# Kernel optimization log

Measured on AMD Instinct MI355X. Metric: run time of the kernel, lower is better.

## Reference

```python
import jax, jax.numpy as jnp
import numpy as np

B, T, N = 4, 24, 512
IN_FT, HID1, HID2, OUT = 64, 64, 64, 64


def _gconv(A, v, W1, W2):
    # two stacked graph-conv layers: relu(A @ v @ W1) then A @ . @ W2 (pre-gate, linear)
    h = jax.nn.relu(jnp.einsum('bij,bjd->bid', A, v) @ W1)   # [B,N,HID2]
    return jnp.einsum('bij,bjd->bid', A, h) @ W2             # [B,N,OUT]


def setup_inputs() -> dict:
    key = jax.random.key(0)
    ks = jax.random.split(key, 10)
    d_in = HID1 + OUT
    def w(k, shape, fan_in):
        return jax.random.normal(k, shape, dtype=jnp.float32) / np.sqrt(fan_in)
    return {
        'x': jax.random.normal(ks[0], (B, T, N, IN_FT), dtype=jnp.float32),
        'e': jax.random.uniform(ks[1], (B, T, N, N, 1), dtype=jnp.float32),
        'fc_w': w(ks[2], (IN_FT, HID1), IN_FT),
        'fc_b': jnp.zeros((HID1,), dtype=jnp.float32),
        'Wz1': w(ks[3], (d_in, HID2), d_in), 'Wz2': w(ks[4], (HID2, OUT), HID2),
        'Wr1': w(ks[5], (d_in, HID2), d_in), 'Wr2': w(ks[6], (HID2, OUT), HID2),
        'Wc1': w(ks[7], (d_in, HID2), d_in), 'Wc2': w(ks[8], (HID2, OUT), HID2),
    }


def reference(x, e, fc_w, fc_b, Wz1, Wz2, Wr1, Wr2, Wc1, Wc2):
    # input projection: relu(Linear(in_ft -> hid_ft1))
    xp = jax.nn.relu(x @ fc_w + fc_b)            # [B,T,N,HID1]
    A = e[..., 0]                                # [B,T,N,N] edge weights
    h0 = jnp.zeros((B, N, OUT), dtype=x.dtype)

    def step(h, inp):
        xt, At = inp                             # [B,N,HID1], [B,N,N]
        xh = jnp.concatenate([xt, h], axis=-1)
        z = jax.nn.sigmoid(_gconv(At, xh, Wz1, Wz2))
        r = jax.nn.sigmoid(_gconv(At, xh, Wr1, Wr2))
        c = jnp.tanh(_gconv(At, jnp.concatenate([xt, r * h], axis=-1), Wc1, Wc2))
        hn = z * h + (1.0 - z) * c
        return hn, hn

    xs = (jnp.moveaxis(xp, 1, 0), jnp.moveaxis(A, 1, 0))  # time-major for scan
    _, hs = jax.lax.scan(step, h0, xs)            # [T,B,N,OUT]
    return jnp.moveaxis(hs, 0, 1)                 # [B,T,N,OUT]
```

## Files before the change

kernel.cpp:

```cpp
#include <hip/hip_runtime.h>
#include <cstdint>
#include <cstddef>

#define B_ 4
#define T_ 24
#define N_ 512

__device__ __forceinline__ float fsig(float x)  { return (float)(1.0 / (1.0 + exp(-(double)x))); }
__device__ __forceinline__ float ftanh(float x) { return (float)tanh((double)x); }

__device__ __forceinline__ int swz16(int f) { return (((f & 15) ^ ((f >> 4) & 15)) << 2); }


__global__ __launch_bounds__(256) void xpT_kernel(const float* __restrict__ x,
                                                  const float* __restrict__ fc_w,
                                                  const float* __restrict__ fc_b,
                                                  float* __restrict__ xpT) {
    __shared__ __align__(16) float sX[64 * 68];
    __shared__ __align__(16) float sW[64 * 64];
    __shared__ float sB[64];
    const int bt = blockIdx.y;
    const int n0 = blockIdx.x * 64;
    const int tid = threadIdx.x;
    for (int i = tid * 4; i < 4096; i += 1024)
        *(float4*)&sW[i] = *(const float4*)&fc_w[i];
    if (tid < 64) sB[tid] = fc_b[tid];
    {
        int r = tid >> 2, kq = (tid & 3) * 16;
        const float* p = x + ((size_t)bt * N_ + n0 + r) * 64 + kq;
        #pragma unroll
        for (int j = 0; j < 4; ++j)
            *(float4*)&sX[r * 68 + kq + j * 4] = *(const float4*)(p + j * 4);
    }
    __syncthreads();
    const int f = tid & 63, ng = tid >> 6;
    float d[16];
    #pragma unroll
    for (int j = 0; j < 16; ++j) d[j] = 0.f;
    for (int k = 0; k < 64; ++k) {
        float w = sW[k * 64 + f];
        #pragma unroll
        for (int j = 0; j < 16; ++j)
            d[j] = fmaf(sX[(ng * 16 + j) * 68 + k], w, d[j]);
    }
    const float bias = sB[f];
    float* o = xpT + ((size_t)bt * 64 + f) * N_ + n0 + ng * 16;
    #pragma unroll
    for (int j = 0; j < 16; ++j)
        o[j] = fmaxf(__fadd_rn(d[j], bias), 0.f);
}

__global__ __launch_bounds__(256) void ux_kernel(const float* __restrict__ e,
                                                 const float* __restrict__ xpT,
                                                 float* __restrict__ UX) {
    __shared__ __align__(16) float sA[2][64 * 72];
    __shared__ __align__(16) float sV[2][64 * 64];
    const int bt = blockIdx.y;
    const int m0 = blockIdx.x * 64;
    const int tid = threadIdx.x;
    const float* Ab = e + ((size_t)bt * N_ + m0) * N_;
    const float* s0 = xpT + (size_t)bt * 64 * N_;

    auto stageA = [&](float* dst, int kt) {
        const int r = tid >> 2, kq = (tid & 3) * 16;
        const float* src = Ab + (size_t)r * N_ + kt * 64 + kq;
        float* d = dst + r * 72 + kq;
        #pragma unroll
        for (int j = 0; j < 4; ++j)
            *(float4*)(d + j * 4) = *(const float4*)(src + j * 4);
    };
    auto stageV = [&](float* dst, int kt) {
        const int f = tid >> 2, q = tid & 3;
        const int sw = swz16(f);
        const float* src = s0 + (size_t)f * N_ + kt * 64;
        #pragma unroll
        for (int j = 0; j < 4; ++j) {
            int k = q * 16 + j * 4;
            *(float4*)&dst[f * 64 + (k ^ sw)] = *(const float4*)(src + k);
        }
    };

    stageA(sA[0], 0);
    stageV(sV[0], 0);
    __syncthreads();

    const int cg = tid & 15, rg = tid >> 4;
    const int c0 = cg * 4;
    float acc[4][4];
    #pragma unroll
    for (int i = 0; i < 4; ++i)
        #pragma unroll
        for (int j = 0; j < 4; ++j) acc[i][j] = 0.f;

    for (int kb = 0; kb < 8; ++kb) {
        if (kb < 7) { stageA(sA[(kb + 1) & 1], kb + 1); stageV(sV[(kb + 1) & 1], kb + 1); }
        const float* Ab_ = sA[kb & 1];
        const float* Vb_ = sV[kb & 1];
        #pragma unroll 4
        for (int kg = 0; kg < 16; ++kg) {
            const int k = kg * 4;
            float4 v[4], a[4];
            #pragma unroll
            for (int j = 0; j < 4; ++j)
                v[j] = *(const float4*)&Vb_[(c0 + j) * 64 + (k ^ swz16(c0 + j))];
            #pragma unroll
            for (int i = 0; i < 4; ++i)
                a[i] = *(const float4*)&Ab_[(rg * 4 + i) * 72 + k];
            #pragma unroll
            for (int i = 0; i < 4; ++i)
                #pragma unroll
                for (int j = 0; j < 4; ++j) {
                    acc[i][j] = fmaf(a[i].x, v[j].x, acc[i][j]);
                    acc[i][j] = fmaf(a[i].y, v[j].y, acc[i][j]);
                    acc[i][j] = fmaf(a[i].z, v[j].z, acc[i][j]);
                    acc[i][j] = fmaf(a[i].w, v[j].w, acc[i][j]);
                }
        }
        __syncthreads();
    }
    #pragma unroll
    for (int i = 0; i < 4; ++i)
        *(float4*)&UX[((size_t)bt * N_ + m0 + rg * 4 + i) * 64 + c0] =
            make_float4(acc[i][0], acc[i][1], acc[i][2], acc[i][3]);
}

template <int STAGE>
__global__ __launch_bounds__(256) void stage9_kernel(
    const float* __restrict__ e, int t,
    const float* __restrict__ UX,
    const float* __restrict__ Wz1, const float* __restrict__ Wz2,
    const float* __restrict__ Wr1, const float* __restrict__ Wr2,
    const float* __restrict__ Wc1, const float* __restrict__ Wc2,
    float* __restrict__ hT, float* __restrict__ hzT, float* __restrict__ hrT,
    float* __restrict__ zT, float* __restrict__ rhT, float* __restrict__ hcT,
    float* __restrict__ out)
{
    constexpr int F = (STAGE == 2) ? 128 : 64;
    constexpr int SC = F + 4;
    __shared__ __align__(16) float sA[8 * 512];
    __shared__ __align__(16) float sV[2 * F * 64];
    __shared__ __align__(16) float sC[8 * SC];
    __shared__ __align__(16) float sUX[8 * 68];

    const int b = blockIdx.y;
    const int m0 = blockIdx.x * 8;
    const int tid = threadIdx.x;
    const int bt = b * T_ + t;

    const float* Ab = e + ((size_t)bt * N_ + m0) * N_;

    const float* s0;
    const float* s1 = nullptr;
    if (STAGE == 1)      { s0 = hT  + (size_t)b * 64 * N_; }
    else if (STAGE == 2) { s0 = hzT + (size_t)b * 64 * N_; s1 = hrT + (size_t)b * 64 * N_; }
    else if (STAGE == 3) { s0 = rhT + (size_t)b * 64 * N_; }
    else                 { s0 = hcT + (size_t)b * 64 * N_; }

    {
        const int r = tid >> 5, seg = (tid & 31) * 16;
        const float* src = Ab + (size_t)r * N_ + seg;
        float* dst = sA + r * 512 + seg;
        #pragma unroll
        for (int j = 0; j < 4; ++j)
            *(float4*)(dst + j * 4) = *(const float4*)(src + j * 4);
    }
    if constexpr (STAGE == 1 || STAGE == 3) {
        if (tid < 128) {
            const int n = tid >> 4, q = (tid & 15) * 4;
            *(float4*)&sUX[n * 68 + q] =
                *(const float4*)&UX[((size_t)bt * N_ + m0 + n) * 64 + q];
        }
    }

    auto stageV = [&](float* dst, int kt) {
        if constexpr (F == 128) {
            const int f = tid >> 1, h = tid & 1;
            const float* src = ((f < 64) ? (s0 + (size_t)f * N_)
                                         : (s1 + (size_t)(f - 64) * N_)) + kt * 64 + h * 32;
            const int sw = swz16(f);
            #pragma unroll
            for (int j = 0; j < 8; ++j)
                *(float4*)&dst[f * 64 + ((h * 32 + j * 4) ^ sw)] = *(const float4*)(src + j * 4);
        } else {
            const int f = tid >> 2, q = tid & 3;
            const float* src = s0 + (size_t)f * N_ + kt * 64 + q * 16;
            const int sw = swz16(f);
            #pragma unroll
            for (int j = 0; j < 4; ++j)
                *(float4*)&dst[f * 64 + ((q * 16 + j * 4) ^ sw)] = *(const float4*)(src + j * 4);
        }
    };

    constexpr int RPT = (F == 128) ? 4 : 2;
    const int c = tid & (F - 1);
    const int rg = (F == 128) ? (tid >> 7) : (tid >> 6);
    const int swc = swz16(c);
    float acc[RPT];
    #pragma unroll
    for (int i = 0; i < RPT; ++i) acc[i] = 0.f;

    stageV(sV, 0);
    __syncthreads();
    for (int kb = 0; kb < 8; ++kb) {
        if (kb < 7) stageV(sV + ((kb + 1) & 1) * (F * 64), kb + 1);
        const float* buf = sV + (kb & 1) * (F * 64);
        #pragma unroll 4
        for (int kg = 0; kg < 16; ++kg) {
            const int k = kg * 4;
            float4 v = *(const float4*)&buf[c * 64 + (k ^ swc)];
            #pragma unroll
            for (int i = 0; i < RPT; ++i) {
                float4 x = *(const float4*)&sA[(rg * RPT + i) * 512 + kb * 64 + k];
                acc[i] = fmaf(x.x, v.x, acc[i]);
                acc[i] = fmaf(x.y, v.y, acc[i]);
                acc[i] = fmaf(x.z, v.z, acc[i]);
                acc[i] = fmaf(x.w, v.w, acc[i]);
            }
        }
        __syncthreads();
    }
    #pragma unroll
    for (int i = 0; i < RPT; ++i)
        sC[(rg * RPT + i) * SC + c] = acc[i];
    __syncthreads();

    if constexpr (STAGE == 1) {
        const int sel = tid >> 7, f = tid & 63, ng = (tid >> 6) & 1, n0 = ng * 4;
        const float* W = sel ? Wr1 : Wz1;
        float d[4] = {0.f, 0.f, 0.f, 0.f};
        #pragma unroll 4
        for (int kq = 0; kq < 16; ++kq) {
            float4 u0 = *(const float4*)&sUX[(n0 + 0) * 68 + kq * 4];
            float4 u1 = *(const float4*)&sUX[(n0 + 1) * 68 + kq * 4];
            float4 u2 = *(const float4*)&sUX[(n0 + 2) * 68 + kq * 4];
            float4 u3 = *(const float4*)&sUX[(n0 + 3) * 68 + kq * 4];
            const float* Wp = W + (kq * 4) * 64 + f;
            float w0 = Wp[0], w1 = Wp[64], w2 = Wp[128], w3 = Wp[192];
            d[0]=fmaf(u0.x,w0,d[0]); d[1]=fmaf(u1.x,w0,d[1]); d[2]=fmaf(u2.x,w0,d[2]); d[3]=fmaf(u3.x,w0,d[3]);
            d[0]=fmaf(u0.y,w1,d[0]); d[1]=fmaf(u1.y,w1,d[1]); d[2]=fmaf(u2.y,w1,d[2]); d[3]=fmaf(u3.y,w1,d[3]);
            d[0]=fmaf(u0.z,w2,d[0]); d[1]=fmaf(u1.z,w2,d[1]); d[2]=fmaf(u2.z,w2,d[2]); d[3]=fmaf(u3.z,w2,d[3]);
            d[0]=fmaf(u0.w,w3,d[0]); d[1]=fmaf(u1.w,w3,d[1]); d[2]=fmaf(u2.w,w3,d[2]); d[3]=fmaf(u3.w,w3,d[3]);
        }
        #pragma unroll 4
        for (int kq = 0; kq < 16; ++kq) {
            float4 c0_ = *(const float4*)&sC[(n0 + 0) * SC + kq * 4];
            float4 c1_ = *(const float4*)&sC[(n0 + 1) * SC + kq * 4];
            float4 c2_ = *(const float4*)&sC[(n0 + 2) * SC + kq * 4];
            float4 c3_ = *(const float4*)&sC[(n0 + 3) * SC + kq * 4];
            const float* Wp = W + (64 + kq * 4) * 64 + f;
            float w0 = Wp[0], w1 = Wp[64], w2 = Wp[128], w3 = Wp[192];
            d[0]=fmaf(c0_.x,w0,d[0]); d[1]=fmaf(c1_.x,w0,d[1]); d[2]=fmaf(c2_.x,w0,d[2]); d[3]=fmaf(c3_.x,w0,d[3]);
            d[0]=fmaf(c0_.y,w1,d[0]); d[1]=fmaf(c1_.y,w1,d[1]); d[2]=fmaf(c2_.y,w1,d[2]); d[3]=fmaf(c3_.y,w1,d[3]);
            d[0]=fmaf(c0_.z,w2,d[0]); d[1]=fmaf(c1_.z,w2,d[1]); d[2]=fmaf(c2_.z,w2,d[2]); d[3]=fmaf(c3_.z,w2,d[3]);
            d[0]=fmaf(c0_.w,w3,d[0]); d[1]=fmaf(c1_.w,w3,d[1]); d[2]=fmaf(c2_.w,w3,d[2]); d[3]=fmaf(c3_.w,w3,d[3]);
        }
        float* dstT = (sel ? hrT : hzT) + (size_t)b * 64 * N_;
        *(float4*)(dstT + (size_t)f * N_ + m0 + n0) =
            make_float4(fmaxf(d[0], 0.f), fmaxf(d[1], 0.f), fmaxf(d[2], 0.f), fmaxf(d[3], 0.f));
    }

    if constexpr (STAGE == 2) {
        const int sel = tid >> 7, f = tid & 63, ng = (tid >> 6) & 1, n0 = ng * 4;
        const float* W = sel ? Wr2 : Wz2;
        const int off = sel * 64;
        float d[4] = {0.f, 0.f, 0.f, 0.f};
        #pragma unroll 4
        for (int kq = 0; kq < 16; ++kq) {
            float4 c0_ = *(const float4*)&sC[(n0 + 0) * SC + off + kq * 4];
            float4 c1_ = *(const float4*)&sC[(n0 + 1) * SC + off + kq * 4];
            float4 c2_ = *(const float4*)&sC[(n0 + 2) * SC + off + kq * 4];
            float4 c3_ = *(const float4*)&sC[(n0 + 3) * SC + off + kq * 4];
            const float* Wp = W + (kq * 4) * 64 + f;
            float w0 = Wp[0], w1 = Wp[64], w2 = Wp[128], w3 = Wp[192];
            d[0]=fmaf(c0_.x,w0,d[0]); d[1]=fmaf(c1_.x,w0,d[1]); d[2]=fmaf(c2_.x,w0,d[2]); d[3]=fmaf(c3_.x,w0,d[3]);
            d[0]=fmaf(c0_.y,w1,d[0]); d[1]=fmaf(c1_.y,w1,d[1]); d[2]=fmaf(c2_.y,w1,d[2]); d[3]=fmaf(c3_.y,w1,d[3]);
            d[0]=fmaf(c0_.z,w2,d[0]); d[1]=fmaf(c1_.z,w2,d[1]); d[2]=fmaf(c2_.z,w2,d[2]); d[3]=fmaf(c3_.z,w2,d[3]);
            d[0]=fmaf(c0_.w,w3,d[0]); d[1]=fmaf(c1_.w,w3,d[1]); d[2]=fmaf(c2_.w,w3,d[2]); d[3]=fmaf(c3_.w,w3,d[3]);
        }
        if (!sel) {
            *(float4*)(zT + ((size_t)b * 64 + f) * N_ + m0 + n0) =
                make_float4(fsig(d[0]), fsig(d[1]), fsig(d[2]), fsig(d[3]));
        } else {
            float4 h4 = *(const float4*)(hT + ((size_t)b * 64 + f) * N_ + m0 + n0);
            *(float4*)(rhT + ((size_t)b * 64 + f) * N_ + m0 + n0) =
                make_float4(__fmul_rn(fsig(d[0]), h4.x), __fmul_rn(fsig(d[1]), h4.y),
                            __fmul_rn(fsig(d[2]), h4.z), __fmul_rn(fsig(d[3]), h4.w));
        }
    }

    if constexpr (STAGE == 3) {
        const int f = tid & 63, ng = tid >> 6, n0 = ng * 2;
        float d[2] = {0.f, 0.f};
        #pragma unroll 4
        for (int kq = 0; kq < 16; ++kq) {
            float4 u0 = *(const float4*)&sUX[(n0 + 0) * 68 + kq * 4];
            float4 u1 = *(const float4*)&sUX[(n0 + 1) * 68 + kq * 4];
            const float* Wp = Wc1 + (kq * 4) * 64 + f;
            float w0 = Wp[0], w1 = Wp[64], w2 = Wp[128], w3 = Wp[192];
            d[0]=fmaf(u0.x,w0,d[0]); d[1]=fmaf(u1.x,w0,d[1]);
            d[0]=fmaf(u0.y,w1,d[0]); d[1]=fmaf(u1.y,w1,d[1]);
            d[0]=fmaf(u0.z,w2,d[0]); d[1]=fmaf(u1.z,w2,d[1]);
            d[0]=fmaf(u0.w,w3,d[0]); d[1]=fmaf(u1.w,w3,d[1]);
        }
        #pragma unroll 4
        for (int kq = 0; kq < 16; ++kq) {
            float4 c0_ = *(const float4*)&sC[(n0 + 0) * SC + kq * 4];
            float4 c1_ = *(const float4*)&sC[(n0 + 1) * SC + kq * 4];
            const float* Wp = Wc1 + (64 + kq * 4) * 64 + f;
            float w0 = Wp[0], w1 = Wp[64], w2 = Wp[128], w3 = Wp[192];
            d[0]=fmaf(c0_.x,w0,d[0]); d[1]=fmaf(c1_.x,w0,d[1]);
            d[0]=fmaf(c0_.y,w1,d[0]); d[1]=fmaf(c1_.y,w1,d[1]);
            d[0]=fmaf(c0_.z,w2,d[0]); d[1]=fmaf(c1_.z,w2,d[1]);
            d[0]=fmaf(c0_.w,w3,d[0]); d[1]=fmaf(c1_.w,w3,d[1]);
        }
        *(float2*)(hcT + ((size_t)b * 64 + f) * N_ + m0 + n0) =
            make_float2(fmaxf(d[0], 0.f), fmaxf(d[1], 0.f));
    }

    if constexpr (STAGE == 4) {
        const int f = tid & 63, ng = tid >> 6, n0 = ng * 2;
        float d[2] = {0.f, 0.f};
        #pragma unroll 4
        for (int kq = 0; kq < 16; ++kq) {
            float4 c0_ = *(const float4*)&sC[(n0 + 0) * SC + kq * 4];
            float4 c1_ = *(const float4*)&sC[(n0 + 1) * SC + kq * 4];
            const float* Wp = Wc2 + (kq * 4) * 64 + f;
            float w0 = Wp[0], w1 = Wp[64], w2 = Wp[128], w3 = Wp[192];
            d[0]=fmaf(c0_.x,w0,d[0]); d[1]=fmaf(c1_.x,w0,d[1]);
            d[0]=fmaf(c0_.y,w1,d[0]); d[1]=fmaf(c1_.y,w1,d[1]);
            d[0]=fmaf(c0_.z,w2,d[0]); d[1]=fmaf(c1_.z,w2,d[1]);
            d[0]=fmaf(c0_.w,w3,d[0]); d[1]=fmaf(c1_.w,w3,d[1]);
        }
        float c0 = ftanh(d[0]), c1 = ftanh(d[1]);
        float* hp = hT + ((size_t)b * 64 + f) * N_ + m0 + n0;
        float2 h2 = *(const float2*)hp;
        float2 z2 = *(const float2*)(zT + ((size_t)b * 64 + f) * N_ + m0 + n0);
        float hn0 = __fadd_rn(__fmul_rn(z2.x, h2.x), __fmul_rn(__fsub_rn(1.f, z2.x), c0));
        float hn1 = __fadd_rn(__fmul_rn(z2.y, h2.y), __fmul_rn(__fsub_rn(1.f, z2.y), c1));
        *(float2*)hp = make_float2(hn0, hn1);
        out[((size_t)bt * N_ + m0 + n0) * 64 + f] = hn0;
        out[((size_t)bt * N_ + m0 + n0 + 1) * 64 + f] = hn1;
    }
    (void)s1;
}


extern "C" void kernel_launch(void* const* d_in, const int* in_sizes, int n_in,
                              void* d_out, int out_size, void* d_ws, size_t ws_size,
                              hipStream_t stream) {
    (void)in_sizes; (void)n_in; (void)out_size; (void)ws_size;
    const float* x    = (const float*)d_in[0];
    const float* e    = (const float*)d_in[1];
    const float* fc_w = (const float*)d_in[2];
    const float* fc_b = (const float*)d_in[3];
    const float* Wz1  = (const float*)d_in[4];
    const float* Wz2  = (const float*)d_in[5];
    const float* Wr1  = (const float*)d_in[6];
    const float* Wr2  = (const float*)d_in[7];
    const float* Wc1  = (const float*)d_in[8];
    const float* Wc2  = (const float*)d_in[9];
    float* out = (float*)d_out;

    char* p = (char*)d_ws;
    auto alloc = [&](size_t bytes) { char* r = p; p += (bytes + 255) & ~(size_t)255; return r; };
    const size_t HSZ = (size_t)B_ * 64 * N_ * 4;
    float* xpT = (float*)alloc((size_t)B_ * T_ * 64 * N_ * 4);
    float* UX  = (float*)alloc((size_t)B_ * T_ * N_ * 64 * 4);
    float* hT  = (float*)alloc(HSZ);
    float* hzT = (float*)alloc(HSZ);
    float* hrT = (float*)alloc(HSZ);
    float* zT  = (float*)alloc(HSZ);
    float* rhT = (float*)alloc(HSZ);
    float* hcT = (float*)alloc(HSZ);

    xpT_kernel<<<dim3(8, B_ * T_), 256, 0, stream>>>(x, fc_w, fc_b, xpT);
    ux_kernel<<<dim3(8, B_ * T_), 256, 0, stream>>>(e, xpT, UX);
    hipMemsetAsync(hT, 0, HSZ, stream);

    dim3 grid(N_ / 8, B_);
    for (int t = 0; t < T_; ++t) {
        stage9_kernel<1><<<grid, 256, 0, stream>>>(e, t, UX, Wz1, Wz2, Wr1, Wr2, Wc1, Wc2,
                                                   hT, hzT, hrT, zT, rhT, hcT, out);
        stage9_kernel<2><<<grid, 256, 0, stream>>>(e, t, UX, Wz1, Wz2, Wr1, Wr2, Wc1, Wc2,
                                                   hT, hzT, hrT, zT, rhT, hcT, out);
        stage9_kernel<3><<<grid, 256, 0, stream>>>(e, t, UX, Wz1, Wz2, Wr1, Wr2, Wc1, Wc2,
                                                   hT, hzT, hrT, zT, rhT, hcT, out);
        stage9_kernel<4><<<grid, 256, 0, stream>>>(e, t, UX, Wz1, Wz2, Wr1, Wr2, Wc1, Wc2,
                                                   hT, hzT, hrT, zT, rhT, hcT, out);
    }
}
```

Measured before the change: 1.734 ms.

## Shrink F=64 stages to 128 threads with 2x2 register tiles

```diff
diff --git a/kernel.cpp b/kernel.cpp
--- a/kernel.cpp
+++ b/kernel.cpp
@@ -125,7 +125,7 @@
 }
 
 template <int STAGE>
-__global__ __launch_bounds__(256) void stage9_kernel(
+__global__ __launch_bounds__((STAGE == 2) ? 256 : 128) void stage_kernel(
     const float* __restrict__ e, int t,
     const float* __restrict__ UX,
     const float* __restrict__ Wz1, const float* __restrict__ Wz2,
@@ -135,7 +135,8 @@
     float* __restrict__ zT, float* __restrict__ rhT, float* __restrict__ hcT,
     float* __restrict__ out)
 {
-    constexpr int F = (STAGE == 2) ? 128 : 64;
+    constexpr int F  = (STAGE == 2) ? 128 : 64;
+    constexpr int NT = (STAGE == 2) ? 256 : 128;
     constexpr int SC = F + 4;
     __shared__ __align__(16) float sA[8 * 512];
     __shared__ __align__(16) float sV[2 * F * 64];
@@ -157,47 +158,45 @@
     else                 { s0 = hcT + (size_t)b * 64 * N_; }
 
     {
-        const int r = tid >> 5, seg = (tid & 31) * 16;
-        const float* src = Ab + (size_t)r * N_ + seg;
-        float* dst = sA + r * 512 + seg;
-        #pragma unroll
-        for (int j = 0; j < 4; ++j)
-            *(float4*)(dst + j * 4) = *(const float4*)(src + j * 4);
+        if constexpr (NT == 256) {
+            const int r = tid >> 5, seg = (tid & 31) * 16;
+            const float* src = Ab + (size_t)r * N_ + seg;
+            float* dst = sA + r * 512 + seg;
+            #pragma unroll
+            for (int j = 0; j < 4; ++j)
+                *(float4*)(dst + j * 4) = *(const float4*)(src + j * 4);
+        } else {
+            const int r = tid >> 4, seg = (tid & 15) * 32;
+            const float* src = Ab + (size_t)r * N_ + seg;
+            float* dst = sA + r * 512 + seg;
+            #pragma unroll
+            for (int j = 0; j < 8; ++j)
+                *(float4*)(dst + j * 4) = *(const float4*)(src + j * 4);
+        }
     }
     if constexpr (STAGE == 1 || STAGE == 3) {
-        if (tid < 128) {
-            const int n = tid >> 4, q = (tid & 15) * 4;
-            *(float4*)&sUX[n * 68 + q] =
-                *(const float4*)&UX[((size_t)bt * N_ + m0 + n) * 64 + q];
-        }
+        const int n = tid >> 4, q = (tid & 15) * 4;
+        *(float4*)&sUX[n * 68 + q] =
+            *(const float4*)&UX[((size_t)bt * N_ + m0 + n) * 64 + q];
     }
 
     auto stageV = [&](float* dst, int kt) {
-        if constexpr (F == 128) {
-            const int f = tid >> 1, h = tid & 1;
-            const float* src = ((f < 64) ? (s0 + (size_t)f * N_)
-                                         : (s1 + (size_t)(f - 64) * N_)) + kt * 64 + h * 32;
-            const int sw = swz16(f);
-            #pragma unroll
-            for (int j = 0; j < 8; ++j)
-                *(float4*)&dst[f * 64 + ((h * 32 + j * 4) ^ sw)] = *(const float4*)(src + j * 4);
-        } else {
-            const int f = tid >> 2, q = tid & 3;
-            const float* src = s0 + (size_t)f * N_ + kt * 64 + q * 16;
-            const int sw = swz16(f);
-            #pragma unroll
-            for (int j = 0; j < 4; ++j)
-                *(float4*)&dst[f * 64 + ((q * 16 + j * 4) ^ sw)] = *(const float4*)(src + j * 4);
-        }
+        const int f = tid >> 1, h = tid & 1;
+        const float* src = ((F == 64 || f < 64) ? (s0 + (size_t)f * N_)
+                                                : (s1 + (size_t)(f - 64) * N_)) + kt * 64 + h * 32;
+        const int sw = swz16(f);
+        #pragma unroll
+        for (int j = 0; j < 8; ++j)
+            *(float4*)&dst[f * 64 + ((h * 32 + j * 4) ^ sw)] = *(const float4*)(src + j * 4);
     };
 
-    constexpr int RPT = (F == 128) ? 4 : 2;
-    const int c = tid & (F - 1);
-    const int rg = (F == 128) ? (tid >> 7) : (tid >> 6);
-    const int swc = swz16(c);
-    float acc[RPT];
-    #pragma unroll
-    for (int i = 0; i < RPT; ++i) acc[i] = 0.f;
+    const int rg = (NT == 256) ? (tid >> 6) : (tid >> 5);
+    const int r0 = 2 * rg;
+    const int cg = (NT == 256) ? (tid & 63) : (tid & 31);
+    const int c0 = (F == 128) ? cg : 2 * cg;
+    const int c1 = (F == 128) ? cg + 64 : 2 * cg + 1;
+    const int sw0 = swz16(c0), sw1 = swz16(c1);
+    float a00 = 0.f, a01 = 0.f, a10 = 0.f, a11 = 0.f;
 
     stageV(sV, 0);
     __syncthreads();
@@ -207,56 +206,68 @@
         #pragma unroll 4
         for (int kg = 0; kg < 16; ++kg) {
             const int k = kg * 4;
-            float4 v = *(const float4*)&buf[c * 64 + (k ^ swc)];
-            #pragma unroll
-            for (int i = 0; i < RPT; ++i) {
-                float4 x = *(const float4*)&sA[(rg * RPT + i) * 512 + kb * 64 + k];
-                acc[i] = fmaf(x.x, v.x, acc[i]);
-                acc[i] = fmaf(x.y, v.y, acc[i]);
-                acc[i] = fmaf(x.z, v.z, acc[i]);
-                acc[i] = fmaf(x.w, v.w, acc[i]);
-            }
+            float4 x0 = *(const float4*)&sA[(r0 + 0) * 512 + kb * 64 + k];
+            float4 x1 = *(const float4*)&sA[(r0 + 1) * 512 + kb * 64 + k];
+            float4 v0 = *(const float4*)&buf[c0 * 64 + (k ^ sw0)];
+            float4 v1 = *(const float4*)&buf[c1 * 64 + (k ^ sw1)];
+            a00 = fmaf(x0.x, v0.x, a00); a00 = fmaf(x0.y, v0.y, a00);
+            a00 = fmaf(x0.z, v0.z, a00); a00 = fmaf(x0.w, v0.w, a00);
+            a01 = fmaf(x0.x, v1.x, a01); a01 = fmaf(x0.y, v1.y, a01);
+            a01 = fmaf(x0.z, v1.z, a01); a01 = fmaf(x0.w, v1.w, a01);
+            a10 = fmaf(x1.x, v0.x, a10); a10 = fmaf(x1.y, v0.y, a10);
+            a10 = fmaf(x1.z, v0.z, a10); a10 = fmaf(x1.w, v0.w, a10);
+            a11 = fmaf(x1.x, v1.x, a11); a11 = fmaf(x1.y, v1.y, a11);
+            a11 = fmaf(x1.z, v1.z, a11); a11 = fmaf(x1.w, v1.w, a11);
         }
         __syncthreads();
     }
-    #pragma unroll
-    for (int i = 0; i < RPT; ++i)
-        sC[(rg * RPT + i) * SC + c] = acc[i];
+    sC[(r0 + 0) * SC + c0] = a00; sC[(r0 + 0) * SC + c1] = a01;
+    sC[(r0 + 1) * SC + c0] = a10; sC[(r0 + 1) * SC + c1] = a11;
     __syncthreads();
 
     if constexpr (STAGE == 1) {
-        const int sel = tid >> 7, f = tid & 63, ng = (tid >> 6) & 1, n0 = ng * 4;
+        const int sel = tid >> 6, f = tid & 63;
         const float* W = sel ? Wr1 : Wz1;
-        float d[4] = {0.f, 0.f, 0.f, 0.f};
-        #pragma unroll 4
-        for (int kq = 0; kq < 16; ++kq) {
-            float4 u0 = *(const float4*)&sUX[(n0 + 0) * 68 + kq * 4];
-            float4 u1 = *(const float4*)&sUX[(n0 + 1) * 68 + kq * 4];
-            float4 u2 = *(const float4*)&sUX[(n0 + 2) * 68 + kq * 4];
-            float4 u3 = *(const float4*)&sUX[(n0 + 3) * 68 + kq * 4];
+        float d[8];
+        #pragma unroll
+        for (int i = 0; i < 8; ++i) d[i] = 0.f;
+        #pragma unroll 4
+        for (int kq = 0; kq < 16; ++kq) {
+            float4 u[8];
+            #pragma unroll
+            for (int i = 0; i < 8; ++i) u[i] = *(const float4*)&sUX[i * 68 + kq * 4];
             const float* Wp = W + (kq * 4) * 64 + f;
             float w0 = Wp[0], w1 = Wp[64], w2 = Wp[128], w3 = Wp[192];
-            d[0]=fmaf(u0.x,w0,d[0]); d[1]=fmaf(u1.x,w0,d[1]); d[2]=fmaf(u2.x,w0,d[2]); d[3]=fmaf(u3.x,w0,d[3]);
-            d[0]=fmaf(u0.y,w1,d[0]); d[1]=fmaf(u1.y,w1,d[1]); d[2]=fmaf(u2.y,w1,d[2]); d[3]=fmaf(u3.y,w1,d[3]);
-            d[0]=fmaf(u0.z,w2,d[0]); d[1]=fmaf(u1.z,w2,d[1]); d[2]=fmaf(u2.z,w2,d[2]); d[3]=fmaf(u3.z,w2,d[3]);
-            d[0]=fmaf(u0.w,w3,d[0]); d[1]=fmaf(u1.w,w3,d[1]); d[2]=fmaf(u2.w,w3,d[2]); d[3]=fmaf(u3.w,w3,d[3]);
-        }
-        #pragma unroll 4
-        for (int kq = 0; kq < 16; ++kq) {
-            float4 c0_ = *(const float4*)&sC[(n0 + 0) * SC + kq * 4];
-            float4 c1_ = *(const float4*)&sC[(n0 + 1) * SC + kq * 4];
-            float4 c2_ = *(const float4*)&sC[(n0 + 2) * SC + kq * 4];
-            float4 c3_ = *(const float4*)&sC[(n0 + 3) * SC + kq * 4];
+            #pragma unroll
+            for (int i = 0; i < 8; ++i) d[i] = fmaf(u[i].x, w0, d[i]);
+            #pragma unroll
+            for (int i = 0; i < 8; ++i) d[i] = fmaf(u[i].y, w1, d[i]);
+            #pragma unroll
+            for (int i = 0; i < 8; ++i) d[i] = fmaf(u[i].z, w2, d[i]);
+            #pragma unroll
+            for (int i = 0; i < 8; ++i) d[i] = fmaf(u[i].w, w3, d[i]);
+        }
+        #pragma unroll 4
+        for (int kq = 0; kq < 16; ++kq) {
+            float4 cv[8];
+            #pragma unroll
+            for (int i = 0; i < 8; ++i) cv[i] = *(const float4*)&sC[i * SC + kq * 4];
             const float* Wp = W + (64 + kq * 4) * 64 + f;
             float w0 = Wp[0], w1 = Wp[64], w2 = Wp[128], w3 = Wp[192];
-            d[0]=fmaf(c0_.x,w0,d[0]); d[1]=fmaf(c1_.x,w0,d[1]); d[2]=fmaf(c2_.x,w0,d[2]); d[3]=fmaf(c3_.x,w0,d[3]);
-            d[0]=fmaf(c0_.y,w1,d[0]); d[1]=fmaf(c1_.y,w1,d[1]); d[2]=fmaf(c2_.y,w1,d[2]); d[3]=fmaf(c3_.y,w1,d[3]);
-            d[0]=fmaf(c0_.z,w2,d[0]); d[1]=fmaf(c1_.z,w2,d[1]); d[2]=fmaf(c2_.z,w2,d[2]); d[3]=fmaf(c3_.z,w2,d[3]);
-            d[0]=fmaf(c0_.w,w3,d[0]); d[1]=fmaf(c1_.w,w3,d[1]); d[2]=fmaf(c2_.w,w3,d[2]); d[3]=fmaf(c3_.w,w3,d[3]);
-        }
-        float* dstT = (sel ? hrT : hzT) + (size_t)b * 64 * N_;
-        *(float4*)(dstT + (size_t)f * N_ + m0 + n0) =
+            #pragma unroll
+            for (int i = 0; i < 8; ++i) d[i] = fmaf(cv[i].x, w0, d[i]);
+            #pragma unroll
+            for (int i = 0; i < 8; ++i) d[i] = fmaf(cv[i].y, w1, d[i]);
+            #pragma unroll
+            for (int i = 0; i < 8; ++i) d[i] = fmaf(cv[i].z, w2, d[i]);
+            #pragma unroll
+            for (int i = 0; i < 8; ++i) d[i] = fmaf(cv[i].w, w3, d[i]);
+        }
+        float* dstT = (sel ? hrT : hzT) + (size_t)b * 64 * N_ + (size_t)f * N_ + m0;
+        *(float4*)(dstT) =
             make_float4(fmaxf(d[0], 0.f), fmaxf(d[1], 0.f), fmaxf(d[2], 0.f), fmaxf(d[3], 0.f));
+        *(float4*)(dstT + 4) =
+            make_float4(fmaxf(d[4], 0.f), fmaxf(d[5], 0.f), fmaxf(d[6], 0.f), fmaxf(d[7], 0.f));
     }
 
     if constexpr (STAGE == 2) {
@@ -289,57 +300,73 @@
     }
 
     if constexpr (STAGE == 3) {
-        const int f = tid & 63, ng = tid >> 6, n0 = ng * 2;
-        float d[2] = {0.f, 0.f};
+        const int w = tid >> 6, f = tid & 63, n0 = w * 4;
+        float d[4] = {0.f, 0.f, 0.f, 0.f};
         #pragma unroll 4
         for (int kq = 0; kq < 16; ++kq) {
             float4 u0 = *(const float4*)&sUX[(n0 + 0) * 68 + kq * 4];
             float4 u1 = *(const float4*)&sUX[(n0 + 1) * 68 + kq * 4];
+            float4 u2 = *(const float4*)&sUX[(n0 + 2) * 68 + kq * 4];
+            float4 u3 = *(const float4*)&sUX[(n0 + 3) * 68 + kq * 4];
             const float* Wp = Wc1 + (kq * 4) * 64 + f;
             float w0 = Wp[0], w1 = Wp[64], w2 = Wp[128], w3 = Wp[192];
-            d[0]=fmaf(u0.x,w0,d[0]); d[1]=fmaf(u1.x,w0,d[1]);
-            d[0]=fmaf(u0.y,w1,d[0]); d[1]=fmaf(u1.y,w1,d[1]);
-            d[0]=fmaf(u0.z,w2,d[0]); d[1]=fmaf(u1.z,w2,d[1]);
-            d[0]=fmaf(u0.w,w3,d[0]); d[1]=fmaf(u1.w,w3,d[1]);
+            d[0]=fmaf(u0.x,w0,d[0]); d[1]=fmaf(u1.x,w0,d[1]); d[2]=fmaf(u2.x,w0,d[2]); d[3]=fmaf(u3.x,w0,d[3]);
+            d[0]=fmaf(u0.y,w1,d[0]); d[1]=fmaf(u1.y,w1,d[1]); d[2]=fmaf(u2.y,w1,d[2]); d[3]=fmaf(u3.y,w1,d[3]);
+            d[0]=fmaf(u0.z,w2,d[0]); d[1]=fmaf(u1.z,w2,d[1]); d[2]=fmaf(u2.z,w2,d[2]); d[3]=fmaf(u3.z,w2,d[3]);
+            d[0]=fmaf(u0.w,w3,d[0]); d[1]=fmaf(u1.w,w3,d[1]); d[2]=fmaf(u2.w,w3,d[2]); d[3]=fmaf(u3.w,w3,d[3]);
         }
         #pragma unroll 4
         for (int kq = 0; kq < 16; ++kq) {
             float4 c0_ = *(const float4*)&sC[(n0 + 0) * SC + kq * 4];
             float4 c1_ = *(const float4*)&sC[(n0 + 1) * SC + kq * 4];
+            float4 c2_ = *(const float4*)&sC[(n0 + 2) * SC + kq * 4];
+            float4 c3_ = *(const float4*)&sC[(n0 + 3) * SC + kq * 4];
             const float* Wp = Wc1 + (64 + kq * 4) * 64 + f;
             float w0 = Wp[0], w1 = Wp[64], w2 = Wp[128], w3 = Wp[192];
-            d[0]=fmaf(c0_.x,w0,d[0]); d[1]=fmaf(c1_.x,w0,d[1]);
-            d[0]=fmaf(c0_.y,w1,d[0]); d[1]=fmaf(c1_.y,w1,d[1]);
-            d[0]=fmaf(c0_.z,w2,d[0]); d[1]=fmaf(c1_.z,w2,d[1]);
-            d[0]=fmaf(c0_.w,w3,d[0]); d[1]=fmaf(c1_.w,w3,d[1]);
-        }
-        *(float2*)(hcT + ((size_t)b * 64 + f) * N_ + m0 + n0) =
-            make_float2(fmaxf(d[0], 0.f), fmaxf(d[1], 0.f));
+            d[0]=fmaf(c0_.x,w0,d[0]); d[1]=fmaf(c1_.x,w0,d[1]); d[2]=fmaf(c2_.x,w0,d[2]); d[3]=fmaf(c3_.x,w0,d[3]);
+            d[0]=fmaf(c0_.y,w1,d[0]); d[1]=fmaf(c1_.y,w1,d[1]); d[2]=fmaf(c2_.y,w1,d[2]); d[3]=fmaf(c3_.y,w1,d[3]);
+            d[0]=fmaf(c0_.z,w2,d[0]); d[1]=fmaf(c1_.z,w2,d[1]); d[2]=fmaf(c2_.z,w2,d[2]); d[3]=fmaf(c3_.z,w2,d[3]);
+            d[0]=fmaf(c0_.w,w3,d[0]); d[1]=fmaf(c1_.w,w3,d[1]); d[2]=fmaf(c2_.w,w3,d[2]); d[3]=fmaf(c3_.w,w3,d[3]);
+        }
+        *(float4*)(hcT + ((size_t)b * 64 + f) * N_ + m0 + n0) =
+            make_float4(fmaxf(d[0], 0.f), fmaxf(d[1], 0.f), fmaxf(d[2], 0.f), fmaxf(d[3], 0.f));
     }
 
     if constexpr (STAGE == 4) {
-        const int f = tid & 63, ng = tid >> 6, n0 = ng * 2;
-        float d[2] = {0.f, 0.f};
+        const int w = tid >> 6, f = tid & 63, n0 = w * 4;
+        float d[4] = {0.f, 0.f, 0.f, 0.f};
         #pragma unroll 4
         for (int kq = 0; kq < 16; ++kq) {
             float4 c0_ = *(const float4*)&sC[(n0 + 0) * SC + kq * 4];
             float4 c1_ = *(const float4*)&sC[(n0 + 1) * SC + kq * 4];
+            float4 c2_ = *(const float4*)&sC[(n0 + 2) * SC + kq * 4];
+            float4 c3_ = *(const float4*)&sC[(n0 + 3) * SC + kq * 4];
             const float* Wp = Wc2 + (kq * 4) * 64 + f;
             float w0 = Wp[0], w1 = Wp[64], w2 = Wp[128], w3 = Wp[192];
-            d[0]=fmaf(c0_.x,w0,d[0]); d[1]=fmaf(c1_.x,w0,d[1]);
-            d[0]=fmaf(c0_.y,w1,d[0]); d[1]=fmaf(c1_.y,w1,d[1]);
-            d[0]=fmaf(c0_.z,w2,d[0]); d[1]=fmaf(c1_.z,w2,d[1]);
-            d[0]=fmaf(c0_.w,w3,d[0]); d[1]=fmaf(c1_.w,w3,d[1]);
-        }
-        float c0 = ftanh(d[0]), c1 = ftanh(d[1]);
+            d[0]=fmaf(c0_.x,w0,d[0]); d[1]=fmaf(c1_.x,w0,d[1]); d[2]=fmaf(c2_.x,w0,d[2]); d[3]=fmaf(c3_.x,w0,d[3]);
+            d[0]=fmaf(c0_.y,w1,d[0]); d[1]=fmaf(c1_.y,w1,d[1]); d[2]=fmaf(c2_.y,w1,d[2]); d[3]=fmaf(c3_.y,w1,d[3]);
+            d[0]=fmaf(c0_.z,w2,d[0]); d[1]=fmaf(c1_.z,w2,d[1]); d[2]=fmaf(c2_.z,w2,d[2]); d[3]=fmaf(c3_.z,w2,d[3]);
+            d[0]=fmaf(c0_.w,w3,d[0]); d[1]=fmaf(c1_.w,w3,d[1]); d[2]=fmaf(c2_.w,w3,d[2]); d[3]=fmaf(c3_.w,w3,d[3]);
+        }
+        float cg0 = ftanh(d[0]), cg1 = ftanh(d[1]), cg2 = ftanh(d[2]), cg3 = ftanh(d[3]);
         float* hp = hT + ((size_t)b * 64 + f) * N_ + m0 + n0;
-        float2 h2 = *(const float2*)hp;
-        float2 z2 = *(const float2*)(zT + ((size_t)b * 64 + f) * N_ + m0 + n0);
-        float hn0 = __fadd_rn(__fmul_rn(z2.x, h2.x), __fmul_rn(__fsub_rn(1.f, z2.x), c0));
-        float hn1 = __fadd_rn(__fmul_rn(z2.y, h2.y), __fmul_rn(__fsub_rn(1.f, z2.y), c1));
-        *(float2*)hp = make_float2(hn0, hn1);
-        out[((size_t)bt * N_ + m0 + n0) * 64 + f] = hn0;
-        out[((size_t)bt * N_ + m0 + n0 + 1) * 64 + f] = hn1;
+        float4 h4 = *(const float4*)hp;
+        float4 z4 = *(const float4*)(zT + ((size_t)b * 64 + f) * N_ + m0 + n0);
+        float hh[4] = {h4.x, h4.y, h4.z, h4.w};
+        float zz[4] = {z4.x, z4.y, z4.z, z4.w};
+        float cc[4] = {cg0, cg1, cg2, cg3};
+        float hn[4];
+        #pragma unroll
+        for (int i = 0; i < 4; ++i) {
+            float t1 = __fmul_rn(zz[i], hh[i]);
+            float om = __fsub_rn(1.0f, zz[i]);
+            float t2 = __fmul_rn(om, cc[i]);
+            hn[i] = __fadd_rn(t1, t2);
+        }
+        *(float4*)hp = make_float4(hn[0], hn[1], hn[2], hn[3]);
+        #pragma unroll
+        for (int i = 0; i < 4; ++i)
+            out[((size_t)bt * N_ + m0 + n0 + i) * 64 + f] = hn[i];
     }
     (void)s1;
 }
@@ -379,13 +406,13 @@
 
     dim3 grid(N_ / 8, B_);
     for (int t = 0; t < T_; ++t) {
-        stage9_kernel<1><<<grid, 256, 0, stream>>>(e, t, UX, Wz1, Wz2, Wr1, Wr2, Wc1, Wc2,
-                                                   hT, hzT, hrT, zT, rhT, hcT, out);
-        stage9_kernel<2><<<grid, 256, 0, stream>>>(e, t, UX, Wz1, Wz2, Wr1, Wr2, Wc1, Wc2,
-                                                   hT, hzT, hrT, zT, rhT, hcT, out);
-        stage9_kernel<3><<<grid, 256, 0, stream>>>(e, t, UX, Wz1, Wz2, Wr1, Wr2, Wc1, Wc2,
-                                                   hT, hzT, hrT, zT, rhT, hcT, out);
-        stage9_kernel<4><<<grid, 256, 0, stream>>>(e, t, UX, Wz1, Wz2, Wr1, Wr2, Wc1, Wc2,
-                                                   hT, hzT, hrT, zT, rhT, hcT, out);
+        stage_kernel<1><<<grid, 128, 0, stream>>>(e, t, UX, Wz1, Wz2, Wr1, Wr2, Wc1, Wc2,
+                                                  hT, hzT, hrT, zT, rhT, hcT, out);
+        stage_kernel<2><<<grid, 256, 0, stream>>>(e, t, UX, Wz1, Wz2, Wr1, Wr2, Wc1, Wc2,
+                                                  hT, hzT, hrT, zT, rhT, hcT, out);
+        stage_kernel<3><<<grid, 128, 0, stream>>>(e, t, UX, Wz1, Wz2, Wr1, Wr2, Wc1, Wc2,
+                                                  hT, hzT, hrT, zT, rhT, hcT, out);
+        stage_kernel<4><<<grid, 128, 0, stream>>>(e, t, UX, Wz1, Wz2, Wr1, Wr2, Wc1, Wc2,
+                                                  hT, hzT, hrT, zT, rhT, hcT, out);
     }
 }
```

Result: slower. 2.031 ms (+17.2%).
